# Optimization experiments

Measured on AMD Instinct MI355X. Metric: run time of the kernel, lower is better.

## Reference

```python
import jax, jax.numpy as jnp
import numpy as np

BN_EPS = 1e-5
ITER_N = 5

def _bn(x, gamma, beta, mean, var, axis):
    shape = [1] * x.ndim
    shape[axis] = -1
    r = lambda v: v.reshape(shape)
    return (x - r(mean)) * (r(gamma) / jnp.sqrt(r(var) + BN_EPS)) + r(beta)

def _covpool(x):
    # x: (B, d, M); MPNCOV CovpoolLayer: y = x @ I_hat @ x^T, I_hat = (1/M)I - (1/M^2)11^T
    M = x.shape[-1]
    I_hat = (-1.0 / (M * M)) * jnp.ones((M, M), x.dtype) + (1.0 / M) * jnp.eye(M, dtype=x.dtype)
    return jnp.einsum('bdm,mn,ben->bde', x, I_hat, x)

def _sqrtm_ns(A, iterN=ITER_N):
    # MPNCOV SqrtmLayer: trace-normalized Newton-Schulz iteration
    d = A.shape[-1]
    I3 = 3.0 * jnp.eye(d, dtype=A.dtype)
    normA = jnp.trace(A, axis1=1, axis2=2) / 3.0          # (B,)
    A_n = A / normA[:, None, None]
    ZY = 0.5 * (I3 - A_n)
    Y = A_n @ ZY
    Z = ZY
    for _ in range(iterN - 2):
        ZY = 0.5 * (I3 - Z @ Y)
        Y = Y @ ZY
        Z = ZY @ Z
    YZY = 0.5 * (Y @ (I3 - Z @ Y))
    return YZY * jnp.sqrt(normA)[:, None, None]

def setup_inputs() -> dict:
    key = jax.random.key(0)
    ks = jax.random.split(key, 12)
    B, C, H, W = 64, 1024, 16, 16
    D, R = 128, H * W  # att_dim, sp_reso
    return {
        'x': jax.random.normal(ks[0], (B, C, H, W), jnp.float32),
        'w_dr': jax.random.normal(ks[1], (D, C), jnp.float32) * 0.02,
        'b_dr': jax.random.normal(ks[2], (D,), jnp.float32) * 0.02,
        'bn1_gamma': jnp.ones((D,), jnp.float32),
        'bn1_beta': jnp.zeros((D,), jnp.float32),
        'bn1_mean': jax.random.normal(ks[3], (D,), jnp.float32) * 0.1,
        'bn1_var': jax.random.uniform(ks[4], (D,), jnp.float32, 0.5, 1.5),
        'bn2_gamma': jnp.ones((R,), jnp.float32),
        'bn2_beta': jnp.zeros((R,), jnp.float32),
        'bn2_mean': jax.random.normal(ks[5], (R,), jnp.float32) * 0.1,
        'bn2_var': jax.random.uniform(ks[6], (R,), jnp.float32, 0.5, 1.5),
        'rc_w': jax.random.normal(ks[7], (R,), jnp.float32) * 0.1 + 1.0,
        'rc_b': jax.random.normal(ks[8], (R,), jnp.float32) * 0.02,
        'fc_w': jax.random.normal(ks[9], (R, R * R), jnp.float32) * 0.004,
        'fc_b': jax.random.normal(ks[10], (R,), jnp.float32) * 0.02,
    }

def reference(x, w_dr, b_dr, bn1_gamma, bn1_beta, bn1_mean, bn1_var,
              bn2_gamma, bn2_beta, bn2_mean, bn2_var, rc_w, rc_b, fc_w, fc_b):
    B, C, H, W = x.shape
    # 1x1 dimension-reduction conv + BN + ReLU
    y = jnp.einsum('bchw,dc->bdhw', x, w_dr) + b_dr[None, :, None, None]
    y = jax.nn.relu(_bn(y, bn1_gamma, bn1_beta, bn1_mean, bn1_var, axis=1))
    # (B, D, HW) -> (B, HW, D): HW spatial positions as 'channels', D as samples
    y = y.reshape(B, -1, H * W).transpose(0, 2, 1)
    cov = _covpool(y)                  # (B, HW, HW)
    s = _sqrtm_ns(cov, ITER_N)         # (B, HW, HW)
    # row BN over first HW axis (channels of the (B, HW, HW, 1) view)
    s = _bn(s, bn2_gamma, bn2_beta, bn2_mean, bn2_var, axis=1)
    # grouped (depthwise) 1x1 row conv: per-row scale + bias
    s = s * rc_w[None, :, None] + rc_b[None, :, None]
    att = jax.nn.sigmoid(s.reshape(B, -1) @ fc_w.T + fc_b)   # (B, HW)
    att = att.reshape(B, 1, H, W)
    return x * att
```

## Files before the change

kernel.cpp:

```cpp
#include <hip/hip_runtime.h>

typedef unsigned short u16;
typedef unsigned int   u32;
typedef __attribute__((ext_vector_type(8))) short bf8;
typedef __attribute__((ext_vector_type(4))) float f4;
typedef __attribute__((ext_vector_type(16))) float f16f;

#define MFMA(a,b,c)   __builtin_amdgcn_mfma_f32_16x16x32_bf16(a,b,c,0,0,0)
#define MFMA32(a,b,c) __builtin_amdgcn_mfma_f32_32x32x16_bf16(a,b,c,0,0,0)

__device__ __forceinline__ u16 f2bf(float f){
  u32 u = __float_as_uint(f);
  u += 0x7fffu + ((u >> 16) & 1u);
  return (u16)(u >> 16);
}
__device__ __forceinline__ float bf2f(u16 h){ return __uint_as_float(((u32)h) << 16); }
__device__ __forceinline__ u32 pk2(float a, float b){ return (u32)f2bf(a) | ((u32)f2bf(b) << 16); }

__device__ __forceinline__ void glds16(const u16* g, u16* l){
  __builtin_amdgcn_global_load_lds((const __attribute__((address_space(1))) u32*)g,
                                   (__attribute__((address_space(3))) u32*)l, 16, 0, 0);
}

__device__ __forceinline__ bf8 ldsFrag(const char* m, int row0, int k0, int pitch){
  int l = threadIdx.x & 63;
  int r = row0 + (l & 15);
  int kb = ((k0 + ((l >> 4) << 3)) << 1) ^ ((r & 7) << 4);
  return *(const bf8*)(m + r * pitch + kb);
}
__device__ __forceinline__ void ldsPut(char* m, int row, int col, int pitch, u16 v){
  int kb = (col << 1) ^ ((row & 7) << 4);
  *(u16*)(m + row * pitch + kb) = v;
}

__device__ __forceinline__ bf8 fragNS(const char* m, int r0, int ks, int l){
  int r = r0 + (l & 31);
  int kb = ((ks << 5) + ((l >> 5) << 4)) ^ ((r & 15) << 4);
  return *(const bf8*)(m + r * 256 + kb);
}
__device__ __forceinline__ bf8 fragWT(const char* m, int r0, int ks, int l){
  int r = r0 + (l & 31);
  int kb = ((ks << 5) + ((l >> 5) << 4)) ^ ((r & 15) << 4);
  return *(const bf8*)(m + r * 512 + kb);
}
__device__ __forceinline__ char* nsAddr(char* m, int row, int col4){
  return m + row * 256 + ((col4 << 1) ^ ((row & 15) << 4));
}

__device__ __forceinline__ void mmPass(const char* A, const char* B, f16f (&acc)[2][2],
                                       int R0, int C0, int l){
  #pragma unroll
  for (int ks = 0; ks < 8; ++ks){
    bf8 a0 = fragNS(A, R0,      ks, l);
    bf8 a1 = fragNS(A, R0 + 32, ks, l);
    bf8 b0 = fragNS(B, C0,      ks, l);
    bf8 b1 = fragNS(B, C0 + 32, ks, l);
    acc[0][0] = MFMA32(a0, b0, acc[0][0]); acc[0][1] = MFMA32(a0, b1, acc[0][1]);
    acc[1][0] = MFMA32(a1, b0, acc[1][0]); acc[1][1] = MFMA32(a1, b1, acc[1][1]);
  }
}

__device__ __forceinline__ void writeTile(char* D, const f16f (&acc)[2][2], int R0, int C0, int l,
                                          float scale, float dval, const uint2* adv){
  #pragma unroll
  for (int ri = 0; ri < 2; ++ri)
  #pragma unroll
  for (int ci = 0; ci < 2; ++ci)
  #pragma unroll
  for (int g = 0; g < 4; ++g){
    int srow = C0 + ci * 32 + (l & 31);
    int scol = R0 + ri * 32 + g * 8 + ((l >> 5) << 2);
    float v[4];
    #pragma unroll
    for (int q = 0; q < 4; ++q){
      float x = scale * acc[ri][ci][g * 4 + q];
      x += ((scol + q) == srow) ? dval : 0.f;
      v[q] = x;
    }
    if (adv){
      uint2 ad = adv[(ri * 2 + ci) * 4 + g];
      v[0] += 1.5f * bf2f((u16)ad.x);
      v[1] += 1.5f * bf2f((u16)(ad.x >> 16));
      v[2] += 1.5f * bf2f((u16)ad.y);
      v[3] += 1.5f * bf2f((u16)(ad.y >> 16));
    }
    *(uint2*)nsAddr(D, srow, scol) = make_uint2(pk2(v[0], v[1]), pk2(v[2], v[3]));
  }
}

__global__ __launch_bounds__(256) void k_prep(const float* __restrict__ wdr,
                                              float* __restrict__ logits,
                                              u16* __restrict__ prep){
  int i = blockIdx.x * 256 + threadIdx.x;
  if (i < 16384) logits[i] = 0.f;
  #pragma unroll
  for (int j = 0; j < 2; ++j){
    int e = i + j * 65536;
    int chunk = e >> 13, rem = e & 8191, d = rem >> 6, cb2 = rem & 63;
    int c = ((cb2 * 2) ^ ((d & 7) << 4)) >> 1;
    prep[e] = f2bf(wdr[d * 1024 + chunk * 64 + c]);
  }
}

__global__ __launch_bounds__(512) void k_conv(
    const u16* __restrict__ wprep, const float* __restrict__ x, const float* __restrict__ bdr,
    const float* __restrict__ g1, const float* __restrict__ be1,
    const float* __restrict__ m1, const float* __restrict__ v1,
    u16* __restrict__ Wg, u16* __restrict__ WTg){
  __shared__ union {
    struct { u16 A[4][8192]; u16 Bt[2][2048]; } s;
    struct { float y[128 * 33]; float musum[512]; float mu[32]; } e;
  } sm;
  int t = threadIdx.x;
  int b = blockIdx.x >> 3, hw0 = (blockIdx.x & 7) * 32;
  const float* xb = x + (size_t)b * 262144 + hw0;

  int w = t >> 6, l = t & 63;
  int d0 = (w >> 1) * 32, hh = (w & 1) * 16;
  int lc = l & 15, lr = (l >> 4) * 4;

  const f4 fz = {0.f, 0.f, 0.f, 0.f};
  f4 acc[2]; acc[0] = fz; acc[1] = fz;

  int cp = t >> 5, hwl = t & 31;
  int bo0 = (4 * cp) ^ ((hwl & 7) << 4);
  int bo1 = (4 * cp + 64) ^ ((hwl & 7) << 4);

  float br[3][4];
  #pragma unroll
  for (int j = 0; j < 3; ++j){
    glds16(wprep + j * 8192 + t * 8,        sm.s.A[j] + t * 8);
    glds16(wprep + j * 8192 + 4096 + t * 8, sm.s.A[j] + 4096 + t * 8);
    __builtin_amdgcn_sched_barrier(0);
    int c0 = j * 64;
    br[j][0] = xb[(size_t)(c0 + 2 * cp)      * 256 + hwl];
    br[j][1] = xb[(size_t)(c0 + 2 * cp + 1)  * 256 + hwl];
    br[j][2] = xb[(size_t)(c0 + 2 * cp + 32) * 256 + hwl];
    br[j][3] = xb[(size_t)(c0 + 2 * cp + 33) * 256 + hwl];
    __builtin_amdgcn_sched_barrier(0);
  }

  #pragma unroll
  for (int k = 0; k < 16; ++k){
    if (k <= 12){
      const u16* src = wprep + (k + 3) * 8192;
      glds16(src + t * 8,        sm.s.A[(k + 3) & 3] + t * 8);
      glds16(src + 4096 + t * 8, sm.s.A[(k + 3) & 3] + 4096 + t * 8);
    }
    __builtin_amdgcn_sched_barrier(0);
    if (k <= 12)      asm volatile("s_waitcnt vmcnt(14)" ::: "memory");
    else if (k == 13) asm volatile("s_waitcnt vmcnt(12)" ::: "memory");
    else if (k == 14) asm volatile("s_waitcnt vmcnt(6)" ::: "memory");
    else              asm volatile("s_waitcnt vmcnt(0)" ::: "memory");
    __builtin_amdgcn_sched_barrier(0);
    *(u32*)((char*)sm.s.Bt[k & 1] + hwl * 128 + bo0) = pk2(br[k % 3][0], br[k % 3][1]);
    *(u32*)((char*)sm.s.Bt[k & 1] + hwl * 128 + bo1) = pk2(br[k % 3][2], br[k % 3][3]);
    __builtin_amdgcn_sched_barrier(0);
    if (k <= 12){
      int c0 = (k + 3) * 64;
      br[k % 3][0] = xb[(size_t)(c0 + 2 * cp)      * 256 + hwl];
      br[k % 3][1] = xb[(size_t)(c0 + 2 * cp + 1)  * 256 + hwl];
      br[k % 3][2] = xb[(size_t)(c0 + 2 * cp + 32) * 256 + hwl];
      br[k % 3][3] = xb[(size_t)(c0 + 2 * cp + 33) * 256 + hwl];
    }
    __builtin_amdgcn_sched_barrier(0);
    asm volatile("s_waitcnt lgkmcnt(0)" ::: "memory");
    __builtin_amdgcn_sched_barrier(0);
    __builtin_amdgcn_s_barrier();
    __builtin_amdgcn_sched_barrier(0);
    #pragma unroll
    for (int ks = 0; ks < 2; ++ks){
      int k0 = ks * 32;
      bf8 a0 = ldsFrag((const char*)sm.s.A[k & 3], d0,      k0, 128);
      bf8 a1 = ldsFrag((const char*)sm.s.A[k & 3], d0 + 16, k0, 128);
      bf8 b0 = ldsFrag((const char*)sm.s.Bt[k & 1], hh, k0, 128);
      acc[0] = MFMA(a0, b0, acc[0]);
      acc[1] = MFMA(a1, b0, acc[1]);
    }
    __builtin_amdgcn_sched_barrier(0);
    __builtin_amdgcn_s_barrier();
    __builtin_amdgcn_sched_barrier(0);
  }
  __syncthreads();

  #pragma unroll
  for (int i = 0; i < 2; ++i)
    #pragma unroll
    for (int r = 0; r < 4; ++r){
      int d = d0 + i * 16 + lr + r;
      float s1 = g1[d] * rsqrtf(v1[d] + 1e-5f);
      float t1 = (bdr[d] - m1[d]) * s1 + be1[d];
      int hwp = hh + lc;
      sm.e.y[d * 33 + hwp] = fmaxf(acc[i][r] * s1 + t1, 0.f);
    }
  __syncthreads();
  { int part = t >> 5, col = t & 31;
    float s = 0.f;
    #pragma unroll
    for (int i2 = 0; i2 < 8; ++i2) s += sm.e.y[(part * 8 + i2) * 33 + col];
    sm.e.musum[part * 32 + col] = s;
  }
  __syncthreads();
  if (t < 32){
    float m = 0.f;
    #pragma unroll
    for (int p = 0; p < 16; ++p) m += sm.e.musum[p * 32 + t];
    sm.e.mu[t] = m * (1.0f / 128.0f);
  }
  __syncthreads();
  const float ISM = 0.08838834764831845f;
  { int hwp = t >> 4, dc = (t & 15) * 8;
    float muv = sm.e.mu[hwp];
    u32 q[4];
    #pragma unroll
    for (int jj = 0; jj < 4; ++jj){
      float a = (sm.e.y[(dc + 2 * jj)     * 33 + hwp] - muv) * ISM;
      float c = (sm.e.y[(dc + 2 * jj + 1) * 33 + hwp] - muv) * ISM;
      q[jj] = pk2(a, c);
    }
    *(uint4*)(Wg + ((size_t)(b * 256 + hw0 + hwp) * 128 + dc)) = make_uint4(q[0], q[1], q[2], q[3]);
  }
  { int d = t >> 2, hc = (t & 3) * 8;
    u32 q[4];
    #pragma unroll
    for (int jj = 0; jj < 4; ++jj){
      int h0 = hc + 2 * jj, h1 = hc + 2 * jj + 1;
      float a = (sm.e.y[d * 33 + h0] - sm.e.mu[h0]) * ISM;
      float c = (sm.e.y[d * 33 + h1] - sm.e.mu[h1]) * ISM;
      q[jj] = pk2(a, c);
    }
    *(uint4*)(WTg + ((size_t)(b * 128 + d) * 256 + hw0 + hc)) = make_uint4(q[0], q[1], q[2], q[3]);
  }
}

extern __shared__ char smns[];
__global__ __launch_bounds__(512, 2) void k_ns(const u16* __restrict__ WT,
                                               u16* __restrict__ yf, float* __restrict__ normAg){
  int b = blockIdx.x, t = threadIdx.x;
  char* Yb = smns;
  char* Zb = smns + 32768;
  char* T1 = smns + 65536;
  char* T2 = smns + 98304;
  char* T3 = smns + 131072;
  char* WTl = smns + 65536;
  char* G   = T3;
  float* trp = (float*)smns;

  int w = t >> 6, l = t & 63;
  int wq = w & 3;
  int R0 = (wq >> 1) * 64, C0 = (wq & 1) * 64;

  { const u16* src = WT + (size_t)b * 32768;
    int row = t >> 2, q = t & 3;
    #pragma unroll
    for (int j = 0; j < 8; ++j) {
      int c16 = q + j * 4;
      bf8 v = *(const bf8*)(src + row * 256 + c16 * 8);
      int ph = c16 ^ (row & 15);
      *(bf8*)(WTl + row * 512 + ph * 16) = v;
    }
  }
  if (t == 0) *trp = 0.f;
  __syncthreads();

  int R0g = (w & 3) * 32, C0g = (w >> 2) * 64;
  const f16f fz16 = {};
  f16f gac[2]; gac[0] = fz16; gac[1] = fz16;
  #pragma unroll
  for (int ks = 0; ks < 16; ++ks){
    bf8 a  = fragWT(WTl, R0g,      ks, l);
    bf8 b0 = fragWT(WTl, C0g,      ks, l);
    bf8 b1 = fragWT(WTl, C0g + 32, ks, l);
    gac[0] = MFMA32(a, b0, gac[0]);
    gac[1] = MFMA32(a, b1, gac[1]);
  }
  float tp = 0.f;
  #pragma unroll
  for (int ci = 0; ci < 2; ++ci)
    #pragma unroll
    for (int e = 0; e < 16; ++e){
      int row = R0g + (e & 3) + 8 * (e >> 2) + ((l >> 5) << 2);
      int col = C0g + ci * 32 + (l & 31);
      if (row == col) tp += gac[ci][e];
    }
  #pragma unroll
  for (int off = 32; off > 0; off >>= 1) tp += __shfl_down(tp, off);
  if (l == 0) atomicAdd(trp, tp);
  __syncthreads();

  float normA = fmaxf(*trp / 3.0f, 1e-12f);
  if (t == 0) normAg[b] = normA;
  float inv = 1.0f / normA;
  #pragma unroll
  for (int ci = 0; ci < 2; ++ci)
    #pragma unroll
    for (int g = 0; g < 4; ++g){
      int srow = C0g + ci * 32 + (l & 31);
      int scol = R0g + g * 8 + ((l >> 5) << 2);
      float v0 = gac[ci][g * 4 + 0] * inv, v1 = gac[ci][g * 4 + 1] * inv;
      float v2 = gac[ci][g * 4 + 2] * inv, v3 = gac[ci][g * 4 + 3] * inv;
      *(uint2*)nsAddr(G, srow, scol) = make_uint2(pk2(v0, v1), pk2(v2, v3));
    }
  __syncthreads();

  bf8 gA[8], gB[8];
  #pragma unroll
  for (int ks = 0; ks < 8; ++ks){
    gA[ks] = fragNS(G, C0,      ks, l);
    gB[ks] = fragNS(G, C0 + 32, ks, l);
  }
  { int row = t >> 2, q4 = t & 3;
    #pragma unroll
    for (int j = 0; j < 4; ++j){
      int c16 = q4 * 4 + j;
      int ph = c16 ^ (row & 15);
      bf8 gg = *(const bf8*)(G + row * 256 + ph * 16);
      bf8 yv, zv;
      #pragma unroll
      for (int e = 0; e < 8; ++e){
        int col = c16 * 8 + e;
        float y = -0.5f * bf2f((u16)gg[e]) + ((col == row) ? 1.5f : 0.f);
        yv[e] = (short)f2bf(y);
        zv[e] = (col == row) ? (short)f2bf(-0.5f) : (short)0;
      }
      *(bf8*)(Yb + row * 256 + ph * 16) = yv;
      *(bf8*)(Zb + row * 256 + ph * 16) = zv;
    }
  }
  __syncthreads();

  float z0 = 1.5f;
  for (int it = 0; it < 4; ++it){
    {
      f16f acc[2][2]; acc[0][0] = fz16; acc[0][1] = fz16; acc[1][0] = fz16; acc[1][1] = fz16;
      const char* As = (w < 4) ? Zb : Yb;
      #pragma unroll
      for (int ks = 0; ks < 8; ++ks){
        bf8 a0 = fragNS(As, R0,      ks, l);
        bf8 a1 = fragNS(As, R0 + 32, ks, l);
        acc[0][0] = MFMA32(a0, gA[ks], acc[0][0]); acc[0][1] = MFMA32(a0, gB[ks], acc[0][1]);
        acc[1][0] = MFMA32(a1, gA[ks], acc[1][0]); acc[1][1] = MFMA32(a1, gB[ks], acc[1][1]);
      }
      writeTile((w < 4) ? T1 : T3, acc, R0, C0, l, 1.0f, (w < 4) ? z0 : 0.f, nullptr);
    }
    __syncthreads();

    uint2 adv[16];
    {
      const char* addsrc = (w < 4) ? Zb : Yb;
      #pragma unroll
      for (int ri = 0; ri < 2; ++ri)
      #pragma unroll
      for (int ci = 0; ci < 2; ++ci)
      #pragma unroll
      for (int g = 0; g < 4; ++g){
        int srow = C0 + ci * 32 + (l & 31);
        int scol = R0 + ri * 32 + g * 8 + ((l >> 5) << 2);
        adv[(ri * 2 + ci) * 4 + g] = *(const uint2*)nsAddr((char*)addsrc, srow, scol);
      }
      int hC0 = C0 + ((w >> 2) << 5);
      f16f a2[2]; a2[0] = fz16; a2[1] = fz16;
      #pragma unroll
      for (int ks = 0; ks < 8; ++ks){
        bf8 a0 = fragNS(T1, R0,      ks, l);
        bf8 a1 = fragNS(T1, R0 + 32, ks, l);
        bf8 b0 = fragNS(Yb, hC0,     ks, l);
        a2[0] = MFMA32(a0, b0, a2[0]);
        a2[1] = MFMA32(a1, b0, a2[1]);
      }
      #pragma unroll
      for (int ri = 0; ri < 2; ++ri)
      #pragma unroll
      for (int g = 0; g < 4; ++g){
        int srow = hC0 + (l & 31);
        int scol = R0 + ri * 32 + g * 8 + ((l >> 5) << 2);
        float v0 = -0.5f * a2[ri][g * 4 + 0], v1 = -0.5f * a2[ri][g * 4 + 1];
        float v2 = -0.5f * a2[ri][g * 4 + 2], v3 = -0.5f * a2[ri][g * 4 + 3];
        *(uint2*)nsAddr(T2, srow, scol) = make_uint2(pk2(v0, v1), pk2(v2, v3));
      }
    }
    __syncthreads();

    if ((w >= 4) || (it < 3)){
      f16f acc[2][2]; acc[0][0] = fz16; acc[0][1] = fz16; acc[1][0] = fz16; acc[1][1] = fz16;
      const char* A3 = (w < 4) ? T2 : T3;
      const char* B3 = (w < 4) ? T1 : T2;
      mmPass(A3, B3, acc, R0, C0, l);
      writeTile((w < 4) ? Zb : Yb, acc, R0, C0, l, 1.0f, 0.f, adv);
    }
    __syncthreads();
    z0 *= 1.5f;
  }

  { int row = t >> 2, q = t & 3;
    u16* dst = yf + (size_t)b * 16384 + row * 128;
    #pragma unroll
    for (int j = 0; j < 4; ++j) {
      int c16 = q * 4 + j;
      int ph = c16 ^ (row & 15);
      *(bf8*)(dst + c16 * 8) = *(const bf8*)(Yb + row * 256 + ph * 16);
    }
  }
}

extern __shared__ char smex[];
__global__ __launch_bounds__(512) void k_expand(
    const u16* __restrict__ Wg, const u16* __restrict__ yf, const float* __restrict__ normAg,
    const float* __restrict__ g2, const float* __restrict__ be2, const float* __restrict__ m2,
    const float* __restrict__ v2, const float* __restrict__ rcw, const float* __restrict__ rcb,
    u16* __restrict__ sp){
  int blk = blockIdx.x, b = blk >> 2, iband = blk & 3;
  char* Bm = smex;
  char* Yl = smex + 65536;
  char* El = smex + 98304;
  int t = threadIdx.x;
  { const u16* src = Wg + (size_t)b * 32768;
    int row = t >> 1, q = t & 1;
    #pragma unroll
    for (int j = 0; j < 8; ++j) {
      int c16 = q + j * 2;
      bf8 v = *(const bf8*)(src + row * 128 + c16 * 8);
      int ph = c16 ^ (row & 7);
      *(bf8*)(Bm + row * 256 + ph * 16) = v;
    } }
  { const u16* src = yf + (size_t)b * 16384;
    int row = t >> 2, q = t & 3;
    #pragma unroll
    for (int j = 0; j < 4; ++j) {
      int c16 = q + j * 4;
      bf8 v = *(const bf8*)(src + row * 128 + c16 * 8);
      int ph = c16 ^ (row & 7);
      *(bf8*)(Yl + row * 256 + ph * 16) = v;
    } }
  __syncthreads();
  int w = t >> 6, l = t & 63, lc = l & 15, lr = (l >> 4) * 4;
  const f4 fz = {0.f, 0.f, 0.f, 0.f};
  { int r0 = (w >> 2) * 32, c0 = (w & 3) * 32;
    f4 acc[2][2];
    acc[0][0] = fz; acc[0][1] = fz; acc[1][0] = fz; acc[1][1] = fz;
    #pragma unroll
    for (int kk = 0; kk < 4; ++kk) {
      int k0 = kk * 32;
      bf8 a0 = ldsFrag(Bm, iband * 64 + r0,      k0, 256);
      bf8 a1 = ldsFrag(Bm, iband * 64 + r0 + 16, k0, 256);
      bf8 b0 = ldsFrag(Yl, c0,      k0, 256);
      bf8 b1 = ldsFrag(Yl, c0 + 16, k0, 256);
      acc[0][0] = MFMA(a0, b0, acc[0][0]); acc[0][1] = MFMA(a0, b1, acc[0][1]);
      acc[1][0] = MFMA(a1, b0, acc[1][0]); acc[1][1] = MFMA(a1, b1, acc[1][1]);
    }
    #pragma unroll
    for (int i = 0; i < 2; ++i)
      #pragma unroll
      for (int j = 0; j < 2; ++j)
        #pragma unroll
        for (int r = 0; r < 4; ++r)
          ldsPut(El, r0 + i * 16 + lr + r, c0 + j * 16 + lc, 256, f2bf(acc[i][j][r]));
  }
  __syncthreads();
  { float invs = rsqrtf(normAg[b]);
    int r0 = (w >> 2) * 32, c0 = (w & 3) * 64;
    f4 acc[2][4];
    #pragma unroll
    for (int i = 0; i < 2; ++i)
      #pragma unroll
      for (int j = 0; j < 4; ++j) acc[i][j] = fz;
    #pragma unroll
    for (int kk = 0; kk < 4; ++kk) {
      int k0 = kk * 32;
      bf8 a0 = ldsFrag(El, r0,      k0, 256);
      bf8 a1 = ldsFrag(El, r0 + 16, k0, 256);
      bf8 b0 = ldsFrag(Bm, c0,      k0, 256);
      bf8 b1 = ldsFrag(Bm, c0 + 16, k0, 256);
      bf8 b2 = ldsFrag(Bm, c0 + 32, k0, 256);
      bf8 b3 = ldsFrag(Bm, c0 + 48, k0, 256);
      acc[0][0] = MFMA(a0, b0, acc[0][0]); acc[0][1] = MFMA(a0, b1, acc[0][1]);
      acc[0][2] = MFMA(a0, b2, acc[0][2]); acc[0][3] = MFMA(a0, b3, acc[0][3]);
      acc[1][0] = MFMA(a1, b0, acc[1][0]); acc[1][1] = MFMA(a1, b1, acc[1][1]);
      acc[1][2] = MFMA(a1, b2, acc[1][2]); acc[1][3] = MFMA(a1, b3, acc[1][3]);
    }
    #pragma unroll
    for (int i = 0; i < 2; ++i)
      #pragma unroll
      for (int r = 0; r < 4; ++r) {
        int il = r0 + i * 16 + lr + r;
        int ig = iband * 64 + il;
        float bs = g2[ig] * rsqrtf(v2[ig] + 1e-5f);
        float al = bs * rcw[ig];
        float be = (be2[ig] - m2[ig] * bs) * rcw[ig] + rcb[ig];
        #pragma unroll
        for (int j = 0; j < 4; ++j) {
          int jg = c0 + j * 16 + lc;
          sp[(size_t)b * 65536 + ig * 256 + jg] = f2bf(acc[i][j][r] * invs * al + be);
        }
      }
  }
}

__global__ __launch_bounds__(256) void k_fc(const u16* __restrict__ sp,
                                            const float* __restrict__ fcw,
                                            float4* __restrict__ partial4){
  __shared__ char Asp[16384];
  __shared__ char Bf[4096];
  int rg = blockIdx.x & 15, kslab = blockIdx.x >> 4;
  int t = threadIdx.x, w = t >> 6, l = t & 63;
  int kbase = kslab * 1024;

  const f4 fz = {0.f, 0.f, 0.f, 0.f};
  f4 acc = fz;

  int frow = t >> 4, fc4 = t & 15;
  const float* fsrc = fcw + (size_t)(rg * 16 + frow) * 65536 + kbase;
  int arow = t >> 2, aq = t & 3;
  const u16* asrc = sp + (size_t)arow * 65536 + kbase;

  for (int c = 0; c < 8; ++c){
    int k0 = c * 128;
    float4 v0 = *(const float4*)(fsrc + k0 + fc4 * 4);
    float4 v1 = *(const float4*)(fsrc + k0 + (fc4 + 16) * 4);
    bf8 av[4];
    #pragma unroll
    for (int j = 0; j < 4; ++j)
      av[j] = *(const bf8*)(asrc + k0 + (aq * 4 + j) * 8);
    {
      int o0 = frow * 256 + (((fc4 >> 1) ^ (frow & 7)) << 4) + ((fc4 & 1) << 3);
      *(uint2*)(Bf + o0) = make_uint2(pk2(v0.x, v0.y), pk2(v0.z, v0.w));
      int c4b = fc4 + 16;
      int o1 = frow * 256 + (((c4b >> 1) ^ (frow & 7)) << 4) + ((c4b & 1) << 3);
      *(uint2*)(Bf + o1) = make_uint2(pk2(v1.x, v1.y), pk2(v1.z, v1.w));
      #pragma unroll
      for (int j = 0; j < 4; ++j){
        int c16 = aq * 4 + j;
        *(bf8*)(Asp + arow * 256 + ((c16 ^ (arow & 7)) << 4)) = av[j];
      }
    }
    __syncthreads();
    #pragma unroll
    for (int ks = 0; ks < 4; ++ks){
      bf8 a = ldsFrag(Asp, w * 16, ks * 32, 256);
      bf8 b = ldsFrag(Bf, 0, ks * 32, 256);
      acc = MFMA(a, b, acc);
    }
    __syncthreads();
  }
  partial4[(size_t)(kslab * 16 + rg) * 256 + t] = make_float4(acc[0], acc[1], acc[2], acc[3]);
}

__global__ __launch_bounds__(256) void k_red(const float4* __restrict__ partial4,
                                             float* __restrict__ logits){
  int rg = blockIdx.x;
  int t = threadIdx.x;
  float4 a = {0,0,0,0};
  #pragma unroll 8
  for (int ks = 0; ks < 64; ++ks){
    float4 v = partial4[(size_t)(ks * 16 + rg) * 256 + t];
    a.x += v.x; a.y += v.y; a.z += v.z; a.w += v.w;
  }
  int w = t >> 6, l = t & 63;
  int brow0 = w * 16 + ((l >> 4) << 2);
  int rcol = rg * 16 + (l & 15);
  float* dst = logits + brow0 * 256 + rcol;
  dst[0]   = a.x;
  dst[256] = a.y;
  dst[512] = a.z;
  dst[768] = a.w;
}

__global__ __launch_bounds__(256) void k_mul(const float* __restrict__ x,
                                             const float* __restrict__ logits,
                                             const float* __restrict__ fcb,
                                             float* __restrict__ out, int n4){
  int i = blockIdx.x * 256 + threadIdx.x;
  int str = gridDim.x * 256;
  for (; i < n4; i += str) {
    int e = i << 2;
    int b = e >> 18;
    int hw = e & 255;
    float4 xv = ((const float4*)x)[i];
    float4 lg = *(const float4*)(logits + (b << 8) + hw);
    float4 fb = *(const float4*)(fcb + hw);
    float4 o;
    o.x = xv.x / (1.f + expf(-(lg.x + fb.x)));
    o.y = xv.y / (1.f + expf(-(lg.y + fb.y)));
    o.z = xv.z / (1.f + expf(-(lg.z + fb.z)));
    o.w = xv.w / (1.f + expf(-(lg.w + fb.w)));
    ((float4*)out)[i] = o;
  }
}

extern "C" void kernel_launch(void* const* d_in, const int* in_sizes, int n_in,
                              void* d_out, int out_size, void* d_ws, size_t ws_size,
                              hipStream_t stream){
  const float* x   = (const float*)d_in[0];
  const float* wdr = (const float*)d_in[1];
  const float* bdr = (const float*)d_in[2];
  const float* g1  = (const float*)d_in[3];
  const float* be1 = (const float*)d_in[4];
  const float* m1  = (const float*)d_in[5];
  const float* v1  = (const float*)d_in[6];
  const float* g2  = (const float*)d_in[7];
  const float* be2 = (const float*)d_in[8];
  const float* m2  = (const float*)d_in[9];
  const float* v2  = (const float*)d_in[10];
  const float* rcw = (const float*)d_in[11];
  const float* rcb = (const float*)d_in[12];
  const float* fcw = (const float*)d_in[13];
  const float* fcb = (const float*)d_in[14];
  float* out = (float*)d_out;
  char* ws = (char*)d_ws;
  u16*    Wg  = (u16*)(ws);
  u16*    WTg = (u16*)(ws + (4u  << 20));
  u16*    yfg = (u16*)(ws + (8u  << 20));
  float*  nAg = (float*)(ws + (10u << 20));
  u16*    wpr = (u16*)(ws + (10u << 20) + 4096);
  u16*    spg = (u16*)(ws + (11u << 20));
  float*  lgt = (float*)(ws + (20u << 20));
  float4* prt = (float4*)(ws + (24u << 20));

  hipFuncSetAttribute((const void*)k_ns,     hipFuncAttributeMaxDynamicSharedMemorySize, 163840);
  hipFuncSetAttribute((const void*)k_expand, hipFuncAttributeMaxDynamicSharedMemorySize, 114688);

  k_prep  <<<256,  256, 0,      stream>>>(wdr, lgt, wpr);
  k_conv  <<<512,  512, 0,      stream>>>(wpr, x, bdr, g1, be1, m1, v1, Wg, WTg);
  k_ns    <<<64,   512, 163840, stream>>>(WTg, yfg, nAg);
  k_expand<<<256,  512, 114688, stream>>>(Wg, yfg, nAg, g2, be2, m2, v2, rcw, rcb, spg);
  k_fc    <<<1024, 256, 0,      stream>>>(spg, fcw, prt);
  k_red   <<<16,   256, 0,      stream>>>(prt, lgt);
  k_mul   <<<2048, 256, 0,      stream>>>(x, lgt, fcb, out, 4194304);
}
```

Before: 113.9 us.

## Double k_ns workgroup to 1024 threads with half-sized per-wave tiles

```diff
diff --git a/kernel.cpp b/kernel.cpp
--- a/kernel.cpp
+++ b/kernel.cpp
@@ -45,47 +45,6 @@
 }
 __device__ __forceinline__ char* nsAddr(char* m, int row, int col4){
   return m + row * 256 + ((col4 << 1) ^ ((row & 15) << 4));
-}
-
-__device__ __forceinline__ void mmPass(const char* A, const char* B, f16f (&acc)[2][2],
-                                       int R0, int C0, int l){
-  #pragma unroll
-  for (int ks = 0; ks < 8; ++ks){
-    bf8 a0 = fragNS(A, R0,      ks, l);
-    bf8 a1 = fragNS(A, R0 + 32, ks, l);
-    bf8 b0 = fragNS(B, C0,      ks, l);
-    bf8 b1 = fragNS(B, C0 + 32, ks, l);
-    acc[0][0] = MFMA32(a0, b0, acc[0][0]); acc[0][1] = MFMA32(a0, b1, acc[0][1]);
-    acc[1][0] = MFMA32(a1, b0, acc[1][0]); acc[1][1] = MFMA32(a1, b1, acc[1][1]);
-  }
-}
-
-__device__ __forceinline__ void writeTile(char* D, const f16f (&acc)[2][2], int R0, int C0, int l,
-                                          float scale, float dval, const uint2* adv){
-  #pragma unroll
-  for (int ri = 0; ri < 2; ++ri)
-  #pragma unroll
-  for (int ci = 0; ci < 2; ++ci)
-  #pragma unroll
-  for (int g = 0; g < 4; ++g){
-    int srow = C0 + ci * 32 + (l & 31);
-    int scol = R0 + ri * 32 + g * 8 + ((l >> 5) << 2);
-    float v[4];
-    #pragma unroll
-    for (int q = 0; q < 4; ++q){
-      float x = scale * acc[ri][ci][g * 4 + q];
-      x += ((scol + q) == srow) ? dval : 0.f;
-      v[q] = x;
-    }
-    if (adv){
-      uint2 ad = adv[(ri * 2 + ci) * 4 + g];
-      v[0] += 1.5f * bf2f((u16)ad.x);
-      v[1] += 1.5f * bf2f((u16)(ad.x >> 16));
-      v[2] += 1.5f * bf2f((u16)ad.y);
-      v[3] += 1.5f * bf2f((u16)(ad.y >> 16));
-    }
-    *(uint2*)nsAddr(D, srow, scol) = make_uint2(pk2(v[0], v[1]), pk2(v[2], v[3]));
-  }
 }
 
 __global__ __launch_bounds__(256) void k_prep(const float* __restrict__ wdr,
@@ -234,8 +193,8 @@
 }
 
 extern __shared__ char smns[];
-__global__ __launch_bounds__(512, 2) void k_ns(const u16* __restrict__ WT,
-                                               u16* __restrict__ yf, float* __restrict__ normAg){
+__global__ __launch_bounds__(1024, 4) void k_ns(const u16* __restrict__ WT,
+                                                u16* __restrict__ yf, float* __restrict__ normAg){
   int b = blockIdx.x, t = threadIdx.x;
   char* Yb = smns;
   char* Zb = smns + 32768;
@@ -247,14 +206,17 @@
   float* trp = (float*)smns;
 
   int w = t >> 6, l = t & 63;
-  int wq = w & 3;
-  int R0 = (wq >> 1) * 64, C0 = (wq & 1) * 64;
-
-  { const u16* src = WT + (size_t)b * 32768;
-    int row = t >> 2, q = t & 3;
-    #pragma unroll
-    for (int j = 0; j < 8; ++j) {
-      int c16 = q + j * 4;
+  int role = w >> 3;
+  int idx = w & 7;
+  int R0  = (idx & 1) * 64;
+  int C0h = (idx >> 1) * 32;
+
+  {
+    const u16* src = WT + (size_t)b * 32768;
+    int row = t >> 3, q = t & 7;
+    #pragma unroll
+    for (int j = 0; j < 4; ++j) {
+      int c16 = q + j * 8;
       bf8 v = *(const bf8*)(src + row * 256 + c16 * 8);
       int ph = c16 ^ (row & 15);
       *(bf8*)(WTl + row * 512 + ph * 16) = v;
@@ -263,26 +225,22 @@
   if (t == 0) *trp = 0.f;
   __syncthreads();
 
-  int R0g = (w & 3) * 32, C0g = (w >> 2) * 64;
+  int R0g = (w & 3) * 32, C0g = (w >> 2) * 32;
   const f16f fz16 = {};
-  f16f gac[2]; gac[0] = fz16; gac[1] = fz16;
+  f16f gac = fz16;
   #pragma unroll
   for (int ks = 0; ks < 16; ++ks){
-    bf8 a  = fragWT(WTl, R0g,      ks, l);
-    bf8 b0 = fragWT(WTl, C0g,      ks, l);
-    bf8 b1 = fragWT(WTl, C0g + 32, ks, l);
-    gac[0] = MFMA32(a, b0, gac[0]);
-    gac[1] = MFMA32(a, b1, gac[1]);
+    bf8 a  = fragWT(WTl, R0g, ks, l);
+    bf8 bb = fragWT(WTl, C0g, ks, l);
+    gac = MFMA32(a, bb, gac);
   }
   float tp = 0.f;
   #pragma unroll
-  for (int ci = 0; ci < 2; ++ci)
-    #pragma unroll
-    for (int e = 0; e < 16; ++e){
-      int row = R0g + (e & 3) + 8 * (e >> 2) + ((l >> 5) << 2);
-      int col = C0g + ci * 32 + (l & 31);
-      if (row == col) tp += gac[ci][e];
-    }
+  for (int e = 0; e < 16; ++e){
+    int row = R0g + (e & 3) + 8 * (e >> 2) + ((l >> 5) << 2);
+    int col = C0g + (l & 31);
+    if (row == col) tp += gac[e];
+  }
   #pragma unroll
   for (int off = 32; off > 0; off >>= 1) tp += __shfl_down(tp, off);
   if (l == 0) atomicAdd(trp, tp);
@@ -292,27 +250,24 @@
   if (t == 0) normAg[b] = normA;
   float inv = 1.0f / normA;
   #pragma unroll
-  for (int ci = 0; ci < 2; ++ci)
-    #pragma unroll
-    for (int g = 0; g < 4; ++g){
-      int srow = C0g + ci * 32 + (l & 31);
-      int scol = R0g + g * 8 + ((l >> 5) << 2);
-      float v0 = gac[ci][g * 4 + 0] * inv, v1 = gac[ci][g * 4 + 1] * inv;
-      float v2 = gac[ci][g * 4 + 2] * inv, v3 = gac[ci][g * 4 + 3] * inv;
-      *(uint2*)nsAddr(G, srow, scol) = make_uint2(pk2(v0, v1), pk2(v2, v3));
-    }
-  __syncthreads();
-
-  bf8 gA[8], gB[8];
-  #pragma unroll
-  for (int ks = 0; ks < 8; ++ks){
-    gA[ks] = fragNS(G, C0,      ks, l);
-    gB[ks] = fragNS(G, C0 + 32, ks, l);
-  }
-  { int row = t >> 2, q4 = t & 3;
-    #pragma unroll
-    for (int j = 0; j < 4; ++j){
-      int c16 = q4 * 4 + j;
+  for (int g = 0; g < 4; ++g){
+    int srow = C0g + (l & 31);
+    int scol = R0g + g * 8 + ((l >> 5) << 2);
+    float v0 = gac[g*4+0]*inv, v1 = gac[g*4+1]*inv;
+    float v2 = gac[g*4+2]*inv, v3 = gac[g*4+3]*inv;
+    *(uint2*)nsAddr(G, srow, scol) = make_uint2(pk2(v0, v1), pk2(v2, v3));
+  }
+  __syncthreads();
+
+  bf8 gA[8];
+  #pragma unroll
+  for (int ks = 0; ks < 8; ++ks) gA[ks] = fragNS(G, C0h, ks, l);
+
+  {
+    int row = t >> 3, q = t & 7;
+    #pragma unroll
+    for (int j = 0; j < 2; ++j){
+      int c16 = q * 2 + j;
       int ph = c16 ^ (row & 15);
       bf8 gg = *(const bf8*)(G + row * 256 + ph * 16);
       bf8 yv, zv;
@@ -332,71 +287,102 @@
   float z0 = 1.5f;
   for (int it = 0; it < 4; ++it){
     {
-      f16f acc[2][2]; acc[0][0] = fz16; acc[0][1] = fz16; acc[1][0] = fz16; acc[1][1] = fz16;
-      const char* As = (w < 4) ? Zb : Yb;
+      f16f acc[2]; acc[0] = fz16; acc[1] = fz16;
+      const char* As = role ? Yb : Zb;
       #pragma unroll
       for (int ks = 0; ks < 8; ++ks){
         bf8 a0 = fragNS(As, R0,      ks, l);
         bf8 a1 = fragNS(As, R0 + 32, ks, l);
-        acc[0][0] = MFMA32(a0, gA[ks], acc[0][0]); acc[0][1] = MFMA32(a0, gB[ks], acc[0][1]);
-        acc[1][0] = MFMA32(a1, gA[ks], acc[1][0]); acc[1][1] = MFMA32(a1, gB[ks], acc[1][1]);
-      }
-      writeTile((w < 4) ? T1 : T3, acc, R0, C0, l, 1.0f, (w < 4) ? z0 : 0.f, nullptr);
+        acc[0] = MFMA32(a0, gA[ks], acc[0]);
+        acc[1] = MFMA32(a1, gA[ks], acc[1]);
+      }
+      char* D = role ? T3 : T1;
+      float dval = role ? 0.f : z0;
+      #pragma unroll
+      for (int ri = 0; ri < 2; ++ri)
+      #pragma unroll
+      for (int g = 0; g < 4; ++g){
+        int srow = C0h + (l & 31);
+        int scol = R0 + ri * 32 + g * 8 + ((l >> 5) << 2);
+        float v[4];
+        #pragma unroll
+        for (int q = 0; q < 4; ++q){
+          float x = acc[ri][g * 4 + q];
+          x += ((scol + q) == srow) ? dval : 0.f;
+          v[q] = x;
+        }
+        *(uint2*)nsAddr(D, srow, scol) = make_uint2(pk2(v[0], v[1]), pk2(v[2], v[3]));
+      }
     }
     __syncthreads();
 
-    uint2 adv[16];
+    uint2 adv[8];
     {
-      const char* addsrc = (w < 4) ? Zb : Yb;
+      const char* addsrc = role ? Yb : Zb;
       #pragma unroll
       for (int ri = 0; ri < 2; ++ri)
       #pragma unroll
-      for (int ci = 0; ci < 2; ++ci)
-      #pragma unroll
       for (int g = 0; g < 4; ++g){
-        int srow = C0 + ci * 32 + (l & 31);
+        int srow = C0h + (l & 31);
         int scol = R0 + ri * 32 + g * 8 + ((l >> 5) << 2);
-        adv[(ri * 2 + ci) * 4 + g] = *(const uint2*)nsAddr((char*)addsrc, srow, scol);
-      }
-      int hC0 = C0 + ((w >> 2) << 5);
-      f16f a2[2]; a2[0] = fz16; a2[1] = fz16;
+        adv[ri * 4 + g] = *(const uint2*)nsAddr((char*)addsrc, srow, scol);
+      }
+      int R2 = (w & 3) * 32, C2 = (w >> 2) * 32;
+      f16f a2 = fz16;
       #pragma unroll
       for (int ks = 0; ks < 8; ++ks){
-        bf8 a0 = fragNS(T1, R0,      ks, l);
-        bf8 a1 = fragNS(T1, R0 + 32, ks, l);
-        bf8 b0 = fragNS(Yb, hC0,     ks, l);
-        a2[0] = MFMA32(a0, b0, a2[0]);
-        a2[1] = MFMA32(a1, b0, a2[1]);
-      }
+        bf8 a0 = fragNS(T1, R2, ks, l);
+        bf8 b0 = fragNS(Yb, C2, ks, l);
+        a2 = MFMA32(a0, b0, a2);
+      }
+      #pragma unroll
+      for (int g = 0; g < 4; ++g){
+        int srow = C2 + (l & 31);
+        int scol = R2 + g * 8 + ((l >> 5) << 2);
+        float v0 = -0.5f * a2[g*4+0], v1 = -0.5f * a2[g*4+1];
+        float v2 = -0.5f * a2[g*4+2], v3 = -0.5f * a2[g*4+3];
+        *(uint2*)nsAddr(T2, srow, scol) = make_uint2(pk2(v0, v1), pk2(v2, v3));
+      }
+    }
+    __syncthreads();
+
+    if (role || (it < 3)){
+      f16f acc[2]; acc[0] = fz16; acc[1] = fz16;
+      const char* A3 = role ? T3 : T2;
+      const char* B3 = role ? T2 : T1;
+      #pragma unroll
+      for (int ks = 0; ks < 8; ++ks){
+        bf8 a0 = fragNS(A3, R0,      ks, l);
+        bf8 a1 = fragNS(A3, R0 + 32, ks, l);
+        bf8 b0 = fragNS(B3, C0h,     ks, l);
+        acc[0] = MFMA32(a0, b0, acc[0]);
+        acc[1] = MFMA32(a1, b0, acc[1]);
+      }
+      char* D = role ? Yb : Zb;
       #pragma unroll
       for (int ri = 0; ri < 2; ++ri)
       #pragma unroll
       for (int g = 0; g < 4; ++g){
-        int srow = hC0 + (l & 31);
+        int srow = C0h + (l & 31);
         int scol = R0 + ri * 32 + g * 8 + ((l >> 5) << 2);
-        float v0 = -0.5f * a2[ri][g * 4 + 0], v1 = -0.5f * a2[ri][g * 4 + 1];
-        float v2 = -0.5f * a2[ri][g * 4 + 2], v3 = -0.5f * a2[ri][g * 4 + 3];
-        *(uint2*)nsAddr(T2, srow, scol) = make_uint2(pk2(v0, v1), pk2(v2, v3));
-      }
-    }
-    __syncthreads();
-
-    if ((w >= 4) || (it < 3)){
-      f16f acc[2][2]; acc[0][0] = fz16; acc[0][1] = fz16; acc[1][0] = fz16; acc[1][1] = fz16;
-      const char* A3 = (w < 4) ? T2 : T3;
-      const char* B3 = (w < 4) ? T1 : T2;
-      mmPass(A3, B3, acc, R0, C0, l);
-      writeTile((w < 4) ? Zb : Yb, acc, R0, C0, l, 1.0f, 0.f, adv);
+        uint2 ad = adv[ri * 4 + g];
+        float v0 = acc[ri][g*4+0] + 1.5f * bf2f((u16)ad.x);
+        float v1 = acc[ri][g*4+1] + 1.5f * bf2f((u16)(ad.x >> 16));
+        float v2 = acc[ri][g*4+2] + 1.5f * bf2f((u16)ad.y);
+        float v3 = acc[ri][g*4+3] + 1.5f * bf2f((u16)(ad.y >> 16));
+        *(uint2*)nsAddr(D, srow, scol) = make_uint2(pk2(v0, v1), pk2(v2, v3));
+      }
     }
     __syncthreads();
     z0 *= 1.5f;
   }
 
-  { int row = t >> 2, q = t & 3;
+  {
+    int row = t >> 3, q = t & 7;
     u16* dst = yf + (size_t)b * 16384 + row * 128;
     #pragma unroll
-    for (int j = 0; j < 4; ++j) {
-      int c16 = q * 4 + j;
+    for (int j = 0; j < 2; ++j) {
+      int c16 = q * 2 + j;
       int ph = c16 ^ (row & 15);
       *(bf8*)(dst + c16 * 8) = *(const bf8*)(Yb + row * 256 + ph * 16);
     }
@@ -621,7 +607,7 @@
 
   k_prep  <<<256,  256, 0,      stream>>>(wdr, lgt, wpr);
   k_conv  <<<512,  512, 0,      stream>>>(wpr, x, bdr, g1, be1, m1, v1, Wg, WTg);
-  k_ns    <<<64,   512, 163840, stream>>>(WTg, yfg, nAg);
+  k_ns    <<<64,   1024, 163840, stream>>>(WTg, yfg, nAg);
   k_expand<<<256,  512, 114688, stream>>>(Wg, yfg, nAg, g2, be2, m2, v2, rcw, rcb, spg);
   k_fc    <<<1024, 256, 0,      stream>>>(spg, fcw, prt);
   k_red   <<<16,   256, 0,      stream>>>(prt, lgt);
```

After: 145.6 us. 1.28x slower.
